# Optimization experiments

Hardware: AMD Instinct MI355X
Metric: run time of the kernel (lower is better)

The kernel has to match this reference:

```python
import jax, jax.numpy as jnp
import numpy as np

EPS = 1e-20  # MaskSoftmax epsilon
S, T, B, H, V = 64, 64, 128, 1024, 32000


def _attn(s, h, u, mask, sa_w, sa_b, a1_w, a1_b):
    # Bahdanau attention with mask-softmax over the source (dim 0)
    t = jnp.tanh(s @ sa_w + sa_b + u)               # [S,B,H]
    e = jnp.einsum('sbh,h->sb', t, a1_w) + a1_b     # [S,B]
    x = jnp.exp(e - jnp.max(e, axis=0, keepdims=True)) * mask
    alpha = x / (jnp.sum(x, axis=0, keepdims=True) + EPS)
    return jnp.einsum('sb,sbh->bh', alpha, h)       # [B,H]


def _gru(x, h, ym, W, U, b, C=None, c=None):
    xg = x @ W + b
    if C is not None:
        xg = xg + c @ C
    hg = h @ U
    xz, xr, xh = jnp.split(xg, 3, axis=-1)
    hz, hr, hh = jnp.split(hg, 3, axis=-1)
    z = jax.nn.sigmoid(xz + hz)
    r = jax.nn.sigmoid(xr + hr)
    hn = (1.0 - z) * h + z * jnp.tanh(xh + r * hh)
    m = ym[:, None]
    return m * hn + (1.0 - m) * h


def _forward(ys, xs_h, uh, xs_mask, ys_mask, s_tm1, emb, sa_w, sa_b, a1_w, a1_b,
             ha_w, ha_b, W1, U1, b1, W2, U2, C2, b2,
             ua1_w, ua1_b, ua2_w, ua2_b, ls_w, ls_b, ly_w, ly_b, lc_w, lc_b):
    ys_e = emb[ys]                                              # [T,B,H]
    btg_uh = jnp.einsum('sbh,hk->sbk', xs_h, ha_w) + ha_b        # [S,B,H]

    def step(s, inp):
        y_e, ym = inp
        s_above = _gru(y_e, s, ym, W1, U1, b1)                   # gru1
        a1 = _attn(s_above, xs_h, uh, xs_mask, sa_w, sa_b, a1_w, a1_b)
        a2 = _attn(s_above, xs_h, btg_uh, xs_mask, sa_w, sa_b, a1_w, a1_b)
        s_t = _gru(a1, s_above, ym, W2, U2, b2, C2, a2)          # gru2 with extra ctx
        g = jax.nn.sigmoid(a1 @ ua1_w + ua1_b + a2 @ ua2_w + ua2_b)
        att = g * a1 + (1.0 - g) * a2                            # gated fusion
        logit = s_t @ ls_w + ls_b + y_e @ ly_w + ly_b + att @ lc_w + lc_b  # [B,2H]
        logit = jnp.max(logit.reshape(logit.shape[0], -1, 2), axis=-1)     # maxout
        return s_t, logit

    _, logits = jax.lax.scan(step, s_tm1, (ys_e, ys_mask))       # [T,B,H]
    return logits * ys_mask[:, :, None]


def setup_inputs():
    key = jax.random.key(0)
    ks = jax.random.split(key, 20)
    rn = lambda k, sh, s=0.02: jax.random.normal(k, sh, jnp.float32) * s
    inp = {}
    inp['ys'] = jax.random.randint(ks[0], (T, B), 0, V)
    inp['xs_h'] = jax.random.normal(ks[1], (S, B, H), jnp.float32)
    inp['uh'] = jax.random.normal(ks[2], (S, B, H), jnp.float32)
    inp['xs_mask'] = jnp.ones((S, B), jnp.float32)
    inp['ys_mask'] = jnp.ones((T, B), jnp.float32)
    inp['s_tm1'] = rn(ks[3], (B, H), 1.0)
    emb = rn(ks[4], (V, H), 1.0)
    inp['emb'] = emb.at[0].set(0.0)  # padding_idx = 0
    inp['sa_w'] = rn(ks[5], (H, H)); inp['sa_b'] = jnp.zeros((H,), jnp.float32)
    inp['a1_w'] = rn(ks[6], (H,));   inp['a1_b'] = jnp.zeros((), jnp.float32)
    inp['ha_w'] = rn(ks[7], (H, H)); inp['ha_b'] = jnp.zeros((H,), jnp.float32)
    inp['W1'] = rn(ks[8], (H, 3 * H)); inp['U1'] = rn(ks[9], (H, 3 * H)); inp['b1'] = jnp.zeros((3 * H,), jnp.float32)
    inp['W2'] = rn(ks[10], (H, 3 * H)); inp['U2'] = rn(ks[11], (H, 3 * H)); inp['C2'] = rn(ks[12], (H, 3 * H)); inp['b2'] = jnp.zeros((3 * H,), jnp.float32)
    inp['ua1_w'] = rn(ks[13], (H, H)); inp['ua1_b'] = jnp.zeros((H,), jnp.float32)
    inp['ua2_w'] = rn(ks[14], (H, H)); inp['ua2_b'] = jnp.zeros((H,), jnp.float32)
    inp['ls_w'] = rn(ks[15], (H, 2 * H)); inp['ls_b'] = jnp.zeros((2 * H,), jnp.float32)
    inp['ly_w'] = rn(ks[16], (H, 2 * H)); inp['ly_b'] = jnp.zeros((2 * H,), jnp.float32)
    inp['lc_w'] = rn(ks[17], (H, 2 * H)); inp['lc_b'] = jnp.zeros((2 * H,), jnp.float32)
    return inp


def reference(ys, xs_h, uh, xs_mask, ys_mask, s_tm1, emb, sa_w, sa_b, a1_w, a1_b,
              ha_w, ha_b, W1, U1, b1, W2, U2, C2, b2,
              ua1_w, ua1_b, ua2_w, ua2_b, ls_w, ls_b, ly_w, ly_b, lc_w, lc_b):
    return _forward(ys, xs_h, uh, xs_mask, ys_mask, s_tm1, emb, sa_w, sa_b, a1_w, a1_b,
                    ha_w, ha_b, W1, U1, b1, W2, U2, C2, b2,
                    ua1_w, ua1_b, ua2_w, ua2_b, ls_w, ls_b, ly_w, ly_b, lc_w, lc_b)
```

## Files before the change

### kernel.cpp

```cpp
#include <hip/hip_runtime.h>
#include <hip/hip_bf16.h>
#include <cstddef>
#include <cstdint>

#define Sdim 64
#define Tdim 64
#define Bdim 128
#define Hdim 1024
#define H3 3072
#define TB (Tdim * Bdim)
#define SB (Sdim * Bdim)
#define NWG 256

typedef __attribute__((ext_vector_type(4))) float f32x4;
typedef __attribute__((ext_vector_type(8))) short bf16x8;

__device__ __forceinline__ float rcpf(float x) { return __builtin_amdgcn_rcpf(x); }
__device__ __forceinline__ float sigf(float x) { return rcpf(1.0f + __expf(-x)); }
__device__ __forceinline__ float tanh_fast(float x) {
  x = fminf(fmaxf(x, -15.0f), 15.0f);
  float t = __expf(2.0f * x);
  return (t - 1.0f) * rcpf(t + 1.0f);
}
__device__ __forceinline__ float bl(uint32_t u) { return __uint_as_float(u << 16); }
__device__ __forceinline__ float bh(uint32_t u) { return __uint_as_float(u & 0xffff0000u); }
__device__ __forceinline__ float b2f(uint16_t v) { return __uint_as_float((uint32_t)v << 16); }
__device__ __forceinline__ uint16_t f2b(float f) {
  __hip_bfloat16 h = __float2bfloat16(f);
  return *reinterpret_cast<uint16_t*>(&h);
}

__device__ __forceinline__ uint32_t ald32(const void* p) {
  return __hip_atomic_load((const uint32_t*)p, __ATOMIC_RELAXED, __HIP_MEMORY_SCOPE_AGENT);
}
__device__ __forceinline__ unsigned long long ald64(const void* p) {
  return __hip_atomic_load((const unsigned long long*)p, __ATOMIC_RELAXED, __HIP_MEMORY_SCOPE_AGENT);
}
__device__ __forceinline__ void ast32(void* p, uint32_t v) {
  __hip_atomic_store((uint32_t*)p, v, __ATOMIC_RELAXED, __HIP_MEMORY_SCOPE_AGENT);
}
__device__ __forceinline__ void ast64(void* p, unsigned long long v) {
  __hip_atomic_store((unsigned long long*)p, v, __ATOMIC_RELAXED, __HIP_MEMORY_SCOPE_AGENT);
}
__device__ __forceinline__ float aldf(const void* p) { return __uint_as_float(ald32(p)); }
__device__ __forceinline__ void astf(void* p, float v) { ast32(p, __float_as_uint(v)); }
__device__ __forceinline__ uint4 ald128(const void* p) {
  unsigned long long a = ald64(p);
  unsigned long long b = ald64((const char*)p + 8);
  uint4 r;
  r.x = (uint32_t)a; r.y = (uint32_t)(a >> 32);
  r.z = (uint32_t)b; r.w = (uint32_t)(b >> 32);
  return r;
}
#define PK2(x, y) ((unsigned long long)__float_as_uint(x) | ((unsigned long long)__float_as_uint(y) << 32))
__device__ __forceinline__ float ulo(unsigned long long u) { return __uint_as_float((uint32_t)u); }
__device__ __forceinline__ float uhi(unsigned long long u) { return __uint_as_float((uint32_t)(u >> 32)); }

struct MDesc {
  const uint16_t* A0; const uint16_t* B0;
  const uint16_t* A1; const uint16_t* B1;
  const uint16_t* A2; const uint16_t* B2;
  const float* bias0; const float* bias1; const float* bias2;
  float* C;
  int M, N, K;
};

template<int BM, int BN, int MODE>
__global__ __launch_bounds__(256) void mgemm(MDesc d, const float* __restrict__ ymask,
                                             float* __restrict__ outp)
{
  const int nb = blockIdx.x * BN;
  const int mb = blockIdx.y * BM;
  if (nb >= d.N || mb >= d.M) return;

  __shared__ char lds[(BM + BN) * 128];
  char* As = lds;
  char* Bs = lds + BM * 128;

  const int t = threadIdx.x;
  const int lane = t & 63;
  const int wid = t >> 6;
  const int wm = wid >> 1, wn = wid & 1;
  constexpr int WM = BM / 2, WN = BN / 2;
  constexpr int MR = WM / 16, NR = WN / 16;
  constexpr int CA = BM / 32;
  constexpr int CB = BN / 32;

  const int arow_base = wm * WM + (lane & 15);
  const int brow_base = wn * WN + (lane & 15);
  const int akb = (lane >> 4) * 16;
  const int axA = (arow_base & 7) << 4;
  const int axB = (brow_base & 7) << 4;

  f32x4 acc[MR][NR];
  #pragma unroll
  for (int m = 0; m < MR; ++m)
    #pragma unroll
    for (int n = 0; n < NR; ++n)
      acc[m][n] = (f32x4){0.f, 0.f, 0.f, 0.f};

  const int K = d.K;
  const int nkt = K / 64;

  #pragma unroll 1
  for (int p = 0; p < 3; ++p) {
    const uint16_t* A = (p == 0) ? d.A0 : (p == 1 ? d.A1 : d.A2);
    const uint16_t* B = (p == 0) ? d.B0 : (p == 1 ? d.B1 : d.B2);
    if (A == nullptr) break;

    const char* gA[CA]; int lA[CA];
    const char* gB[CB]; int lB[CB];
    #pragma unroll
    for (int c = 0; c < CA; ++c) {
      int i = c * 256 + t, row = i >> 3, kb = (i & 7) * 16;
      gA[c] = (const char*)A + (size_t)(mb + row) * K * 2 + kb;
      lA[c] = row * 128 + (kb ^ ((row & 7) << 4));
    }
    #pragma unroll
    for (int c = 0; c < CB; ++c) {
      int i = c * 256 + t, row = i >> 3, kb = (i & 7) * 16;
      gB[c] = (const char*)B + (size_t)(nb + row) * K * 2 + kb;
      lB[c] = row * 128 + (kb ^ ((row & 7) << 4));
    }

    uint4 ra[CA], rb[CB];
    #pragma unroll
    for (int c = 0; c < CA; ++c) ra[c] = *(const uint4*)gA[c];
    #pragma unroll
    for (int c = 0; c < CB; ++c) rb[c] = *(const uint4*)gB[c];

    for (int kk = 0; kk < nkt; ++kk) {
      __syncthreads();
      #pragma unroll
      for (int c = 0; c < CA; ++c) *(uint4*)(As + lA[c]) = ra[c];
      #pragma unroll
      for (int c = 0; c < CB; ++c) *(uint4*)(Bs + lB[c]) = rb[c];
      __syncthreads();
      if (kk + 1 < nkt) {
        #pragma unroll
        for (int c = 0; c < CA; ++c) ra[c] = *(const uint4*)(gA[c] + (size_t)(kk + 1) * 128);
        #pragma unroll
        for (int c = 0; c < CB; ++c) rb[c] = *(const uint4*)(gB[c] + (size_t)(kk + 1) * 128);
      }
      #pragma unroll
      for (int ks = 0; ks < 2; ++ks) {
        bf16x8 av[MR], bv[NR];
        #pragma unroll
        for (int m = 0; m < MR; ++m) {
          int row = arow_base + m * 16;
          av[m] = *(const bf16x8*)(As + row * 128 + ((ks * 64 + akb) ^ axA));
        }
        #pragma unroll
        for (int n = 0; n < NR; ++n) {
          int row = brow_base + n * 16;
          bv[n] = *(const bf16x8*)(Bs + row * 128 + ((ks * 64 + akb) ^ axB));
        }
        #pragma unroll
        for (int m = 0; m < MR; ++m)
          #pragma unroll
          for (int n = 0; n < NR; ++n)
            acc[m][n] = __builtin_amdgcn_mfma_f32_16x16x32_bf16(av[m], bv[n], acc[m][n], 0, 0, 0);
      }
    }
  }

  const int cm = (lane >> 4) * 4;
  const int cn = lane & 15;
  #pragma unroll
  for (int n = 0; n < NR; ++n) {
    int col = nb + wn * WN + n * 16 + cn;
    float bias = 0.f;
    if (d.bias0) bias += d.bias0[col];
    if (d.bias1) bias += d.bias1[col];
    if (d.bias2) bias += d.bias2[col];
    #pragma unroll
    for (int m = 0; m < MR; ++m) {
      #pragma unroll
      for (int j = 0; j < 4; ++j) {
        int row = mb + wm * WM + m * 16 + cm + j;
        float v = acc[m][n][j] + bias;
        if (MODE == 1) {
          ((uint16_t*)d.C)[(size_t)row * d.N + col] = f2b(v);
        } else {
          float o = __shfl_xor(v, 1);
          if (!(lane & 1))
            outp[(size_t)row * (d.N / 2) + (col >> 1)] = fmaxf(v, o) * ymask[row];
        }
      }
    }
  }
}

static inline MDesc mk(const uint16_t* A0, const uint16_t* B0,
                       const uint16_t* A1, const uint16_t* B1,
                       const uint16_t* A2, const uint16_t* B2,
                       const float* b0, const float* b1, const float* b2,
                       float* C, int M, int N, int K)
{
  MDesc d;
  d.A0 = A0; d.B0 = B0; d.A1 = A1; d.B1 = B1; d.A2 = A2; d.B2 = B2;
  d.bias0 = b0; d.bias1 = b1; d.bias2 = b2;
  d.C = C; d.M = M; d.N = N; d.K = K;
  return d;
}

__global__ __launch_bounds__(256) void transpose_bf16_k(const float* __restrict__ in,
                                                        uint16_t* __restrict__ out,
                                                        int K, int N)
{
  __shared__ float tile[32][33];
  int nx = blockIdx.x * 32, ky = blockIdx.y * 32;
  int tx = threadIdx.x & 31, ty = threadIdx.x >> 5;
  #pragma unroll
  for (int i = 0; i < 4; ++i)
    tile[ty + i * 8][tx] = in[(size_t)(ky + ty + i * 8) * N + nx + tx];
  __syncthreads();
  #pragma unroll
  for (int i = 0; i < 4; ++i)
    out[(size_t)(nx + ty + i * 8) * K + ky + tx] = f2b(tile[tx][ty + i * 8]);
}

__global__ __launch_bounds__(256) void ptranspose_k(const float* __restrict__ in,
                                                    uint16_t* __restrict__ out,
                                                    int K, int N)
{
  __shared__ float tile[32][33];
  int nx = blockIdx.x * 32, ky = blockIdx.y * 32;
  int tx = threadIdx.x & 31, ty = threadIdx.x >> 5;
  #pragma unroll
  for (int i = 0; i < 4; ++i)
    tile[ty + i * 8][tx] = in[(size_t)(ky + ty + i * 8) * N + nx + tx];
  __syncthreads();
  #pragma unroll
  for (int i = 0; i < 4; ++i) {
    int n = nx + ty + i * 8;
    int h = n & 1023, g = n >> 10;
    int np = (h >> 4) * 48 + g * 16 + (h & 15);
    out[(size_t)np * K + ky + tx] = f2b(tile[tx][ty + i * 8]);
  }
}

__global__ __launch_bounds__(256) void pack_k(const float* __restrict__ b1,
                                              const float* __restrict__ b2,
                                              float* __restrict__ b1p,
                                              float* __restrict__ b2p,
                                              int* __restrict__ bar)
{
  int i = blockIdx.x * 256 + threadIdx.x;
  if (i < 1024) bar[i] = 0;
  if (i < H3) {
    int g = (i >> 4) % 3, hblk = i / 48, hi = i & 15;
    int n = g * 1024 + hblk * 16 + hi;
    b1p[i] = b1[n];
    b2p[i] = b2[n];
  }
}

__global__ __launch_bounds__(256) void cvt_bf16_k(const float* __restrict__ in,
                                                  uint16_t* __restrict__ out)
{
  int gid = blockIdx.x * 256 + threadIdx.x;
  float4 v = ((const float4*)in)[gid];
  uint2 o;
  o.x = (uint32_t)f2b(v.x) | ((uint32_t)f2b(v.y) << 16);
  o.y = (uint32_t)f2b(v.z) | ((uint32_t)f2b(v.w) << 16);
  ((uint2*)out)[gid] = o;
}

__global__ __launch_bounds__(256) void embed_k(const int* __restrict__ ys,
                                               const float* __restrict__ emb,
                                               uint16_t* __restrict__ ys_e)
{
  int gid = blockIdx.x * 256 + threadIdx.x;
  int h4 = gid & 255;
  int tb = gid >> 8;
  int tok = ys[tb];
  float4 v = ((const float4*)emb)[(size_t)tok * 256 + h4];
  uint2 o;
  o.x = (uint32_t)f2b(v.x) | ((uint32_t)f2b(v.y) << 16);
  o.y = (uint32_t)f2b(v.z) | ((uint32_t)f2b(v.w) << 16);
  ((uint2*)ys_e)[gid] = o;
}

struct ScanArgs {
  const uint16_t *U1p, *W2p, *C2p, *U2p;
  const uint16_t *sawt, *ua1t, *ua2t;
  const uint16_t *xw1p;
  const uint16_t *uh_bf, *btg_bf, *xs_bf;
  const uint16_t *stm1_bf;
  const float *s_tm1, *ys_mask, *xs_mask, *a1w, *a1b, *sa_b;
  const float *b2p, *ua1_b, *ua2_b;
  float *sf0, *sf1, *sab_f, *qbuf, *e1, *e2, *c1f, *c2f, *ahg;
  float *p1part, *p5part;
  uint16_t *sab_bf, *c1b, *c2b, *shist_bf, *att_bf;
  int *bar;
};

__device__ __forceinline__ void gsync(int* bar, int gen, int wg) {
  __syncthreads();
  if (threadIdx.x == 0) {
    asm volatile("s_waitcnt vmcnt(0)" ::: "memory");
    int old = __hip_atomic_fetch_add(bar + (wg & 15) * 32, 1,
                                     __ATOMIC_RELAXED, __HIP_MEMORY_SCOPE_AGENT);
    if (old == gen * 16 - 1) {
      int ro = __hip_atomic_fetch_add(bar + 512, 1,
                                      __ATOMIC_RELAXED, __HIP_MEMORY_SCOPE_AGENT);
      if (ro == gen * 16 - 1)
        __hip_atomic_store(bar + 544, gen, __ATOMIC_RELAXED, __HIP_MEMORY_SCOPE_AGENT);
    }
    while (__hip_atomic_load(bar + 544, __ATOMIC_RELAXED, __HIP_MEMORY_SCOPE_AGENT) < gen)
      __builtin_amdgcn_s_sleep(2);
    asm volatile("s_waitcnt vmcnt(0)" ::: "memory");
  }
  __syncthreads();
}

#define HS1 16384
#define HS2 12288
#define HS6 16384
#define HS5 32768


__global__ __launch_bounds__(256, 1) void scan2_k(ScanArgs a) {
  const int wg = blockIdx.x;
  const int t = threadIdx.x;
  const int lane = t & 63, w = t >> 6;
  const int r15 = lane & 15;
  const int akb = (lane >> 4) * 16;
  __shared__ char lds[64 * 1024];
  int gen = 0;

  float wv[16];
  {
    const float* wp = a.a1w + lane * 16;
    #pragma unroll
    for (int j = 0; j < 16; ++j) wv[j] = wp[j];
  }
  const float abv = a.a1b[0];

  const int b34 = wg & 127;
  const uint16_t* src34 = (wg < 128) ? a.uh_bf : a.btg_bf;
  const size_t s34_base = ((size_t)(w * 16) * Bdim + b34) * 1024 + lane * 16;
  float* cf34 = (wg < 128) ? a.c1f : a.c2f;
  uint16_t* cb34 = (wg < 128) ? a.c1b : a.c2b;
  const uint16_t* xp34 = a.xs_bf + (size_t)b34 * 1024 + t * 4;

  const int bh6 = (wg & 127) >> 6, hb6 = wg & 63;
  const char* ga6[4]; int la6[4];
  {
    #pragma unroll
    for (int c = 0; c < 4; ++c) {
      int i = c * 256 + t;
      int row = i >> 3, kb = (i & 7) * 16;
      if (i < 512) {
        ga6[c] = (const char*)a.sab_bf + ((size_t)(bh6 * 64 + row) * 1024) * 2 + kb;
      } else if (i < 896) {
        int j2 = i - 512; int row2 = j2 >> 3;
        ga6[c] = (const char*)a.U2p + ((size_t)(hb6 * 48 + row2) * 1024) * 2 + kb;
        row = 64 + row2;
      } else {
        ga6[c] = (const char*)a.U2p + kb;
      }
      la6[c] = row * 128 + (kb ^ ((row & 7) << 4));
    }
  }

  const int bh5 = (wg & 127) >> 6, hblk = wg & 63;
  const int pairid = wg & 127;
  const int koff = (wg < 128) ? 0 : 8;

  const char* ga5[8]; int la5[8];
  {
    #pragma unroll
    for (int c = 0; c < 8; ++c) {
      int i = c * 256 + t;
      int kb = (i & 7) * 16, grow = i >> 3;
      const char* gp;
      if (grow < 64)       gp = (const char*)a.c1b  + ((size_t)(bh5 * 64 + grow)        * 1024) * 2;
      else if (grow < 128) gp = (const char*)a.c2b  + ((size_t)(bh5 * 64 + grow - 64)   * 1024) * 2;
      else if (grow < 176) gp = (const char*)a.W2p  + ((size_t)(hblk * 48 + grow - 128) * 1024) * 2;
      else if (grow < 224) gp = (const char*)a.C2p  + ((size_t)(hblk * 48 + grow - 176) * 1024) * 2;
      else if (grow < 240) gp = (const char*)a.ua1t + ((size_t)(hblk * 16 + grow - 224) * 1024) * 2;
      else                 gp = (const char*)a.ua2t + ((size_t)(hblk * 16 + grow - 240) * 1024) * 2;
      ga5[c] = gp + kb + (size_t)koff * 128;
      la5[c] = grow * 128 + (kb ^ ((grow & 7) << 4));
    }
  }

  unsigned long long* p1p = (unsigned long long*)a.p1part + (size_t)pairid * 1536 + t;
  unsigned long long* p5p = (unsigned long long*)a.p5part + (size_t)pairid * 2048 + t;

  for (int step = 0; step < Tdim; ++step) {
    const uint16_t* sprev_bf = step ? (a.shist_bf + (size_t)(step - 1) * Bdim * Hdim) : a.stm1_bf;
    const float* sprev_f = (step == 0) ? a.s_tm1 : ((step & 1) ? a.sf0 : a.sf1);
    float* snext_f = (step & 1) ? a.sf1 : a.sf0;
    const float* ymt = a.ys_mask + (size_t)step * Bdim;
    uint16_t* shist_t = a.shist_bf + (size_t)step * Bdim * Hdim;
    uint16_t* att_t = a.att_bf + (size_t)step * Bdim * Hdim;
    const uint16_t* xw1t = a.xw1p + (size_t)step * Bdim * H3;

    {
      const char* ga1[4]; int la1[4];
      #pragma unroll
      for (int c = 0; c < 4; ++c) {
        int i = c * 256 + t;
        int row = i >> 3, kb = (i & 7) * 16;
        if (i < 512) {
          ga1[c] = (const char*)sprev_bf + ((size_t)(bh5 * 64 + row) * 1024) * 2 + kb;
        } else if (i < 896) {
          int j2 = i - 512; int row2 = j2 >> 3;
          ga1[c] = (const char*)a.U1p + ((size_t)(hblk * 48 + row2) * 1024) * 2 + kb;
          row = 64 + row2;
        } else {
          ga1[c] = (const char*)a.U1p + kb;
        }
        ga1[c] += (size_t)koff * 128;
        la1[c] = row * 128 + (kb ^ ((row & 7) << 4));
      }
      f32x4 ac0 = {0.f,0.f,0.f,0.f}, ac1 = ac0, ac2 = ac0;
      const int arow = w * 16 + r15;
      const int axA = (arow & 7) << 4;
      const int axB = (r15 & 7) << 4;
      uint4 rA[4], rB[4];
      auto ld1 = [&](uint4* r, int tile) {
        #pragma unroll
        for (int c = 0; c < 4; ++c)
          r[c] = (c < 2) ? ald128(ga1[c] + (size_t)tile * 128)
                         : *(const uint4*)(ga1[c] + (size_t)tile * 128);
      };
      auto st1 = [&](const uint4* r, int half) {
        char* base = lds + half * HS1;
        #pragma unroll
        for (int c = 0; c < 4; ++c) *(uint4*)(base + la1[c]) = r[c];
      };
      auto cp1 = [&](int half) {
        const char* base = lds + half * HS1;
        #pragma unroll
        for (int ks = 0; ks < 2; ++ks) {
          int ko = ks * 64 + akb;
          bf16x8 av = *(const bf16x8*)(base + arow * 128 + (ko ^ axA));
          bf16x8 b0 = *(const bf16x8*)(base + (64 + r15) * 128 + (ko ^ axB));
          bf16x8 b1 = *(const bf16x8*)(base + (80 + r15) * 128 + (ko ^ axB));
          bf16x8 b2 = *(const bf16x8*)(base + (96 + r15) * 128 + (ko ^ axB));
          ac0 = __builtin_amdgcn_mfma_f32_16x16x32_bf16(av, b0, ac0, 0, 0, 0);
          ac1 = __builtin_amdgcn_mfma_f32_16x16x32_bf16(av, b1, ac1, 0, 0, 0);
          ac2 = __builtin_amdgcn_mfma_f32_16x16x32_bf16(av, b2, ac2, 0, 0, 0);
        }
      };
      ld1(rA, 0); ld1(rB, 1);
      st1(rA, 0);
      #pragma unroll 1
      for (int kk2 = 0; kk2 < 4; ++kk2) {
        __syncthreads();
        st1(rB, 1);
        if (kk2 < 3) ld1(rA, 2 * kk2 + 2);
        cp1(0);
        __syncthreads();
        if (kk2 < 3) { st1(rA, 0); ld1(rB, 2 * kk2 + 3); }
        cp1(1);
      }
      if (wg >= 128) {
        ast64(p1p +    0, PK2(ac0[0], ac0[1]));
        ast64(p1p +  256, PK2(ac0[2], ac0[3]));
        ast64(p1p +  512, PK2(ac1[0], ac1[1]));
        ast64(p1p +  768, PK2(ac1[2], ac1[3]));
        ast64(p1p + 1024, PK2(ac2[0], ac2[1]));
        ast64(p1p + 1280, PK2(ac2[2], ac2[3]));
        __syncthreads();
        if (t == 0)
          __hip_atomic_store(a.bar + 600 + pairid, step + 1,
                             __ATOMIC_RELAXED, __HIP_MEMORY_SCOPE_AGENT);
      } else {
        if (t == 0) {
          while (__hip_atomic_load(a.bar + 600 + pairid,
                                   __ATOMIC_RELAXED, __HIP_MEMORY_SCOPE_AGENT) < step + 1)
            __builtin_amdgcn_s_sleep(1);
        }
        __syncthreads();
        unsigned long long u0 = ald64(p1p), u1 = ald64(p1p + 256),
                           u2 = ald64(p1p + 512), u3 = ald64(p1p + 768),
                           u4 = ald64(p1p + 1024), u5 = ald64(p1p + 1280);
        ac0[0] += ulo(u0); ac0[1] += uhi(u0); ac0[2] += ulo(u1); ac0[3] += uhi(u1);
        ac1[0] += ulo(u2); ac1[1] += uhi(u2); ac1[2] += ulo(u3); ac1[3] += uhi(u3);
        ac2[0] += ulo(u4); ac2[1] += uhi(u4); ac2[2] += ulo(u5); ac2[3] += uhi(u5);
        const int hgl = hblk * 16 + r15;
        const int bbase = bh5 * 64 + w * 16 + ((lane >> 4) << 2);
        #pragma unroll
        for (int j = 0; j < 4; ++j) {
          int b = bbase + j;
          size_t xr_ = (size_t)b * H3 + hblk * 48 + r15;
          float xz = b2f(xw1t[xr_]);
          float xr = b2f(xw1t[xr_ + 16]);
          float xh = b2f(xw1t[xr_ + 32]);
          float hp = aldf(sprev_f + b * 1024 + hgl);
          float z = sigf(xz + ac0[j]);
          float r = sigf(xr + ac1[j]);
          float hn = (1.f - z) * hp + z * tanh_fast(xh + r * ac2[j]);
          float m = ymt[b];
          float o = m * hn + (1.f - m) * hp;
          astf(a.sab_f + b * 1024 + hgl, o);
          uint32_t me = f2b(o);
          uint32_t other = (uint32_t)__shfl_xor((int)me, 1);
          if (!(lane & 1))
            ast32((char*)a.sab_bf + ((size_t)b * 1024 + hgl) * 2, me | (other << 16));
        }
      }
    }
    gsync(a.bar, ++gen, wg);

    if (wg < 64) {
      const int bh2 = wg >> 5, nblk = wg & 31;
      const char* ga2[3]; int la2[3];
      #pragma unroll
      for (int c = 0; c < 3; ++c) {
        int i = c * 256 + t;
        int row, kb = (i & 7) * 16;
        if (i < 512) {
          row = i >> 3;
          ga2[c] = (const char*)a.sab_bf + ((size_t)(bh2 * 64 + row) * 1024) * 2 + kb;
        } else {
          int j2 = i - 512; int row2 = j2 >> 3;
          ga2[c] = (const char*)a.sawt + ((size_t)(nblk * 32 + row2) * 1024) * 2 + kb;
          row = 64 + row2;
        }
        la2[c] = row * 128 + (kb ^ ((row & 7) << 4));
      }
      f32x4 q0 = {0.f,0.f,0.f,0.f}, q1 = q0;
      const int arow = w * 16 + r15;
      const int axA = (arow & 7) << 4;
      const int axB = (r15 & 7) << 4;
      uint4 rA[3], rB[3];
      auto ld2 = [&](uint4* r, int tile) {
        #pragma unroll
        for (int c = 0; c < 3; ++c)
          r[c] = (c < 2) ? ald128(ga2[c] + (size_t)tile * 128)
                         : *(const uint4*)(ga2[c] + (size_t)tile * 128);
      };
      auto st2 = [&](const uint4* r, int half) {
        char* base = lds + half * HS2;
        #pragma unroll
        for (int c = 0; c < 3; ++c) *(uint4*)(base + la2[c]) = r[c];
      };
      auto cp2 = [&](int half) {
        const char* base = lds + half * HS2;
        #pragma unroll
        for (int ks = 0; ks < 2; ++ks) {
          int ko = ks * 64 + akb;
          bf16x8 av = *(const bf16x8*)(base + arow * 128 + (ko ^ axA));
          bf16x8 b0 = *(const bf16x8*)(base + (64 + r15) * 128 + (ko ^ axB));
          bf16x8 b1 = *(const bf16x8*)(base + (80 + r15) * 128 + (ko ^ axB));
          q0 = __builtin_amdgcn_mfma_f32_16x16x32_bf16(av, b0, q0, 0, 0, 0);
          q1 = __builtin_amdgcn_mfma_f32_16x16x32_bf16(av, b1, q1, 0, 0, 0);
        }
      };
      ld2(rA, 0); ld2(rB, 1);
      st2(rA, 0);
      #pragma unroll 1
      for (int kk2 = 0; kk2 < 8; ++kk2) {
        __syncthreads();
        st2(rB, 1);
        if (kk2 < 7) ld2(rA, 2 * kk2 + 2);
        cp2(0);
        __syncthreads();
        if (kk2 < 7) { st2(rA, 0); ld2(rB, 2 * kk2 + 3); }
        cp2(1);
      }
      #pragma unroll
      for (int n = 0; n < 2; ++n) {
        int col = nblk * 32 + n * 16 + r15;
        float sb = a.sa_b[col];
        #pragma unroll
        for (int j = 0; j < 4; ++j) {
          int b = bh2 * 64 + w * 16 + ((lane >> 4) << 2) + j;
          astf(a.qbuf + b * 1024 + col, (n ? q1[j] : q0[j]) + sb);
        }
      }
    } else if (wg >= 128) {
      f32x4 ac0 = {0.f,0.f,0.f,0.f}, ac1 = ac0, ac2 = ac0;
      const int arow = w * 16 + r15;
      const int axA = (arow & 7) << 4;
      const int axB = (r15 & 7) << 4;
      uint4 rA[4], rB[4];
      auto ld6 = [&](uint4* r, int tile) {
        #pragma unroll
        for (int c = 0; c < 4; ++c)
          r[c] = (c < 2) ? ald128(ga6[c] + (size_t)tile * 128)
                         : *(const uint4*)(ga6[c] + (size_t)tile * 128);
      };
      auto st6 = [&](const uint4* r, int half) {
        char* base = lds + half * HS6;
        #pragma unroll
        for (int c = 0; c < 4; ++c) *(uint4*)(base + la6[c]) = r[c];
      };
      auto cp6 = [&](int half) {
        const char* base = lds + half * HS6;
        #pragma unroll
        for (int ks = 0; ks < 2; ++ks) {
          int ko = ks * 64 + akb;
          bf16x8 av = *(const bf16x8*)(base + arow * 128 + (ko ^ axA));
          bf16x8 b0 = *(const bf16x8*)(base + (64 + r15) * 128 + (ko ^ axB));
          bf16x8 b1 = *(const bf16x8*)(base + (80 + r15) * 128 + (ko ^ axB));
          bf16x8 b2 = *(const bf16x8*)(base + (96 + r15) * 128 + (ko ^ axB));
          ac0 = __builtin_amdgcn_mfma_f32_16x16x32_bf16(av, b0, ac0, 0, 0, 0);
          ac1 = __builtin_amdgcn_mfma_f32_16x16x32_bf16(av, b1, ac1, 0, 0, 0);
          ac2 = __builtin_amdgcn_mfma_f32_16x16x32_bf16(av, b2, ac2, 0, 0, 0);
        }
      };
      ld6(rA, 0); ld6(rB, 1);
      st6(rA, 0);
      #pragma unroll 1
      for (int kk2 = 0; kk2 < 8; ++kk2) {
        __syncthreads();
        st6(rB, 1);
        if (kk2 < 7) ld6(rA, 2 * kk2 + 2);
        cp6(0);
        __syncthreads();
        if (kk2 < 7) { st6(rA, 0); ld6(rB, 2 * kk2 + 3); }
        cp6(1);
      }
      const int bbase6 = bh6 * 64 + w * 16 + ((lane >> 4) << 2);
      #pragma unroll
      for (int j = 0; j < 4; ++j) {
        int b = bbase6 + j;
        float* ap = a.ahg + (size_t)b * H3 + hb6 * 48 + r15;
        astf(ap, ac0[j]);
        astf(ap + 16, ac1[j]);
        astf(ap + 32, ac2[j]);
      }
    }
    uint4 pa0 = *(const uint4*)(src34 + s34_base);
    uint4 pa1 = *(const uint4*)(src34 + s34_base + 8);
    gsync(a.bar, ++gen, wg);

    {
      float* e_lds = (float*)lds;
      float qv[16];
      const float* qp = a.qbuf + (size_t)b34 * 1024 + lane * 16;
      #pragma unroll
      for (int k2 = 0; k2 < 8; ++k2) {
        unsigned long long q2 = ald64(qp + k2 * 2);
        qv[2 * k2]     = __uint_as_float((uint32_t)q2);
        qv[2 * k2 + 1] = __uint_as_float((uint32_t)(q2 >> 32));
      }
      auto score = [&](uint4 u0, uint4 u1, int si) {
        float pv = 0.f;
        uint32_t uu[8] = {u0.x,u0.y,u0.z,u0.w,u1.x,u1.y,u1.z,u1.w};
        #pragma unroll
        for (int k = 0; k < 8; ++k) {
          pv += wv[2*k]   * tanh_fast(qv[2*k]   + bl(uu[k]));
          pv += wv[2*k+1] * tanh_fast(qv[2*k+1] + bh(uu[k]));
        }
        #pragma unroll
        for (int off = 32; off > 0; off >>= 1) pv += __shfl_xor(pv, off);
        if (lane == 0) e_lds[w * 16 + si] = pv + abv;
      };
      uint4 pb0, pb1;
      {
        const uint16_t* np = src34 + s34_base + (size_t)Bdim * 1024;
        pb0 = *(const uint4*)np; pb1 = *(const uint4*)(np + 8);
      }
      #pragma unroll 1
      for (int s2 = 0; s2 < 8; ++s2) {
        {
          int si = 2 * s2;
          uint4 u0 = pa0, u1 = pa1;
          if (s2 < 7) {
            const uint16_t* np = src34 + s34_base + (size_t)(si + 2) * Bdim * 1024;
            pa0 = *(const uint4*)np; pa1 = *(const uint4*)(np + 8);
          }
          score(u0, u1, si);
        }
        {
          int si = 2 * s2 + 1;
          uint4 u0 = pb0, u1 = pb1;
          if (s2 < 7) {
            const uint16_t* np = src34 + s34_base + (size_t)(si + 2) * Bdim * 1024;
            pb0 = *(const uint4*)np; pb1 = *(const uint4*)(np + 8);
          }
          score(u0, u1, si);
        }
      }
      __syncthreads();
      if (w == 0) {
        float vv = e_lds[lane];
        float mx = vv;
        #pragma unroll
        for (int off = 32; off > 0; off >>= 1) mx = fmaxf(mx, __shfl_xor(mx, off));
        float x = __expf(vv - mx) * a.xs_mask[lane * Bdim + b34];
        float sm = x;
        #pragma unroll
        for (int off = 32; off > 0; off >>= 1) sm += __shfl_xor(sm, off);
        e_lds[lane] = x * rcpf(sm + 1e-20f);
      }
      __syncthreads();
      float s0 = 0.f, s1 = 0.f, s2 = 0.f, s3 = 0.f;
      #pragma unroll 8
      for (int s = 0; s < Sdim; ++s) {
        unsigned long long u = *(const unsigned long long*)(xp34 + (size_t)s * Bdim * 1024);
        float aa = e_lds[s];
        s0 += aa * bl((uint32_t)u);
        s1 += aa * bh((uint32_t)u);
        s2 += aa * bl((uint32_t)(u >> 32));
        s3 += aa * bh((uint32_t)(u >> 32));
      }
      size_t o = (size_t)b34 * 1024 + t * 4;
      ast64(cf34 + o,     (unsigned long long)__float_as_uint(s0)
                        | ((unsigned long long)__float_as_uint(s1) << 32));
      ast64(cf34 + o + 2, (unsigned long long)__float_as_uint(s2)
                        | ((unsigned long long)__float_as_uint(s3) << 32));
      unsigned long long pb = (unsigned long long)f2b(s0)
                            | ((unsigned long long)f2b(s1) << 16)
                            | ((unsigned long long)f2b(s2) << 32)
                            | ((unsigned long long)f2b(s3) << 48);
      ast64((char*)cb34 + o * 2, pb);
    }
    uint4 v5w[8];
    {
      #pragma unroll
      for (int c = 4; c < 8; ++c) {
        v5w[c - 4] = *(const uint4*)ga5[c];
        v5w[c]     = *(const uint4*)(ga5[c] + 128);
      }
    }
    gsync(a.bar, ++gen, wg);

    {
      f32x4 ax0 = {0.f,0.f,0.f,0.f}, ax1 = ax0, ax2 = ax0, ag = ax0;
      uint4 rA[8], rB[8];
      auto ld5 = [&](uint4* r, int tile) {
        #pragma unroll
        for (int c = 0; c < 8; ++c)
          r[c] = (c < 4) ? ald128(ga5[c] + (size_t)tile * 128)
                         : *(const uint4*)(ga5[c] + (size_t)tile * 128);
      };
      auto st5 = [&](const uint4* r, int half) {
        char* base = lds + half * HS5;
        #pragma unroll
        for (int c = 0; c < 8; ++c) *(uint4*)(base + la5[c]) = r[c];
      };
      auto cp5 = [&](int half) {
        const char* base = lds + half * HS5;
        #pragma unroll
        for (int ks = 0; ks < 2; ++ks) {
          const int ko = ks * 64 + akb;
          #define LD(row_) (*(const bf16x8*)(base + (row_) * 128 + (ko ^ (((row_) & 7) << 4))))
          bf16x8 a1v = LD(w * 16 + r15);
          bf16x8 a2v = LD(64 + w * 16 + r15);
          bf16x8 bw0 = LD(128 + r15), bw1 = LD(144 + r15), bw2 = LD(160 + r15);
          bf16x8 bc0 = LD(176 + r15), bc1 = LD(192 + r15), bc2 = LD(208 + r15);
          bf16x8 g1v = LD(224 + r15), g2v = LD(240 + r15);
          #undef LD
          ax0 = __builtin_amdgcn_mfma_f32_16x16x32_bf16(a1v, bw0, ax0, 0, 0, 0);
          ax0 = __builtin_amdgcn_mfma_f32_16x16x32_bf16(a2v, bc0, ax0, 0, 0, 0);
          ax1 = __builtin_amdgcn_mfma_f32_16x16x32_bf16(a1v, bw1, ax1, 0, 0, 0);
          ax1 = __builtin_amdgcn_mfma_f32_16x16x32_bf16(a2v, bc1, ax1, 0, 0, 0);
          ax2 = __builtin_amdgcn_mfma_f32_16x16x32_bf16(a1v, bw2, ax2, 0, 0, 0);
          ax2 = __builtin_amdgcn_mfma_f32_16x16x32_bf16(a2v, bc2, ax2, 0, 0, 0);
          ag  = __builtin_amdgcn_mfma_f32_16x16x32_bf16(a1v, g1v, ag, 0, 0, 0);
          ag  = __builtin_amdgcn_mfma_f32_16x16x32_bf16(a2v, g2v, ag, 0, 0, 0);
        }
      };
      #pragma unroll
      for (int c = 0; c < 4; ++c) {
        rA[c] = ald128(ga5[c]);
        rB[c] = ald128(ga5[c] + 128);
      }
      #pragma unroll
      for (int c = 4; c < 8; ++c) { rA[c] = v5w[c - 4]; rB[c] = v5w[c]; }
      st5(rA, 0);
      #pragma unroll 1
      for (int kk2 = 0; kk2 < 4; ++kk2) {
        __syncthreads();
        st5(rB, 1);
        if (kk2 < 3) ld5(rA, 2 * kk2 + 2);
        cp5(0);
        __syncthreads();
        if (kk2 < 3) { st5(rA, 0); ld5(rB, 2 * kk2 + 3); }
        cp5(1);
      }
      if (wg >= 128) {
        ast64(p5p +    0, PK2(ax0[0], ax0[1]));
        ast64(p5p +  256, PK2(ax0[2], ax0[3]));
        ast64(p5p +  512, PK2(ax1[0], ax1[1]));
        ast64(p5p +  768, PK2(ax1[2], ax1[3]));
        ast64(p5p + 1024, PK2(ax2[0], ax2[1]));
        ast64(p5p + 1280, PK2(ax2[2], ax2[3]));
        ast64(p5p + 1536, PK2(ag[0], ag[1]));
        ast64(p5p + 1792, PK2(ag[2], ag[3]));
        __syncthreads();
        if (t == 0)
          __hip_atomic_store(a.bar + 728 + pairid, step + 1,
                             __ATOMIC_RELAXED, __HIP_MEMORY_SCOPE_AGENT);
      } else {
        if (t == 0) {
          while (__hip_atomic_load(a.bar + 728 + pairid,
                                   __ATOMIC_RELAXED, __HIP_MEMORY_SCOPE_AGENT) < step + 1)
            __builtin_amdgcn_s_sleep(1);
        }
        __syncthreads();
        unsigned long long u0 = ald64(p5p), u1 = ald64(p5p + 256),
                           u2 = ald64(p5p + 512), u3 = ald64(p5p + 768),
                           u4 = ald64(p5p + 1024), u5 = ald64(p5p + 1280),
                           u6 = ald64(p5p + 1536), u7 = ald64(p5p + 1792);
        ax0[0] += ulo(u0); ax0[1] += uhi(u0); ax0[2] += ulo(u1); ax0[3] += uhi(u1);
        ax1[0] += ulo(u2); ax1[1] += uhi(u2); ax1[2] += ulo(u3); ax1[3] += uhi(u3);
        ax2[0] += ulo(u4); ax2[1] += uhi(u4); ax2[2] += ulo(u5); ax2[3] += uhi(u5);
        ag[0]  += ulo(u6); ag[1]  += uhi(u6); ag[2]  += ulo(u7); ag[3]  += uhi(u7);
        const int hgl = hblk * 16 + r15;
        float bz  = a.b2p[hblk * 48 + r15];
        float brr = a.b2p[hblk * 48 + 16 + r15];
        float bhh = a.b2p[hblk * 48 + 32 + r15];
        float gb  = a.ua1_b[hgl] + a.ua2_b[hgl];
        const int bbase = bh5 * 64 + w * 16 + ((lane >> 4) << 2);
        float ahz[4], ahr[4], ahh[4], hpv[4], c1v[4], c2v[4];
        #pragma unroll
        for (int j = 0; j < 4; ++j) {
          int b = bbase + j;
          const float* ap = a.ahg + (size_t)b * H3 + hblk * 48 + r15;
          ahz[j] = aldf(ap);
          ahr[j] = aldf(ap + 16);
          ahh[j] = aldf(ap + 32);
          hpv[j] = aldf(a.sab_f + (size_t)b * 1024 + hgl);
          c1v[j] = aldf(a.c1f + (size_t)b * 1024 + hgl);
          c2v[j] = aldf(a.c2f + (size_t)b * 1024 + hgl);
        }
        #pragma unroll
        for (int j = 0; j < 4; ++j) {
          int b = bbase + j;
          float hp = hpv[j];
          float z = sigf(ax0[j] + bz + ahz[j]);
          float r = sigf(ax1[j] + brr + ahr[j]);
          float hn = (1.f - z) * hp + z * tanh_fast(ax2[j] + bhh + r * ahh[j]);
          float m = ymt[b];
          float st = m * hn + (1.f - m) * hp;
          astf(snext_f + b * 1024 + hgl, st);
          uint32_t me = f2b(st);
          uint32_t other = (uint32_t)__shfl_xor((int)me, 1);
          if (!(lane & 1))
            ast32((char*)shist_t + ((size_t)b * 1024 + hgl) * 2, me | (other << 16));
          float g = sigf(ag[j] + gb);
          float att = g * c1v[j] + (1.f - g) * c2v[j];
          att_t[(size_t)b * 1024 + hgl] = f2b(att);
        }
      }
    }
    gsync(a.bar, ++gen, wg);
  }
}

extern "C" void kernel_launch(void* const* d_in, const int* in_sizes, int n_in,
                              void* d_out, int out_size, void* d_ws, size_t ws_size,
                              hipStream_t stream)
{
  const int*   ys      = (const int*)  d_in[0];
  const float* xs_h    = (const float*)d_in[1];
  const float* uh      = (const float*)d_in[2];
  const float* xs_mask = (const float*)d_in[3];
  const float* ys_mask = (const float*)d_in[4];
  const float* s_tm1   = (const float*)d_in[5];
  const float* emb     = (const float*)d_in[6];
  const float* sa_w    = (const float*)d_in[7];
  const float* sa_b    = (const float*)d_in[8];
  const float* a1_w    = (const float*)d_in[9];
  const float* a1_b    = (const float*)d_in[10];
  const float* ha_w    = (const float*)d_in[11];
  const float* ha_b    = (const float*)d_in[12];
  const float* W1      = (const float*)d_in[13];
  const float* U1      = (const float*)d_in[14];
  const float* b1      = (const float*)d_in[15];
  const float* W2      = (const float*)d_in[16];
  const float* U2      = (const float*)d_in[17];
  const float* C2      = (const float*)d_in[18];
  const float* b2      = (const float*)d_in[19];
  const float* ua1_w   = (const float*)d_in[20];
  const float* ua1_b   = (const float*)d_in[21];
  const float* ua2_w   = (const float*)d_in[22];
  const float* ua2_b   = (const float*)d_in[23];
  const float* ls_w    = (const float*)d_in[24];
  const float* ls_b    = (const float*)d_in[25];
  const float* ly_w    = (const float*)d_in[26];
  const float* ly_b    = (const float*)d_in[27];
  const float* lc_w    = (const float*)d_in[28];
  const float* lc_b    = (const float*)d_in[29];
  (void)in_sizes; (void)n_in; (void)out_size; (void)ws_size;

  float* out = (float*)d_out;

  char* wp = (char*)d_ws;
  auto alloc = [&](size_t bytes) { char* r = wp; wp += (bytes + 255) & ~(size_t)255; return r; };

  uint16_t* W1p  = (uint16_t*)alloc((size_t)H3 * Hdim * 2);
  uint16_t* U1p  = (uint16_t*)alloc((size_t)H3 * Hdim * 2);
  uint16_t* W2p  = (uint16_t*)alloc((size_t)H3 * Hdim * 2);
  uint16_t* U2p  = (uint16_t*)alloc((size_t)H3 * Hdim * 2);
  uint16_t* C2p  = (uint16_t*)alloc((size_t)H3 * Hdim * 2);
  uint16_t* sawt = (uint16_t*)alloc((size_t)Hdim * Hdim * 2);
  uint16_t* hawt = (uint16_t*)alloc((size_t)Hdim * Hdim * 2);
  uint16_t* ua1t = (uint16_t*)alloc((size_t)Hdim * Hdim * 2);
  uint16_t* ua2t = (uint16_t*)alloc((size_t)Hdim * Hdim * 2);
  uint16_t* lst  = (uint16_t*)alloc((size_t)2048 * Hdim * 2);
  uint16_t* lyt  = (uint16_t*)alloc((size_t)2048 * Hdim * 2);
  uint16_t* lct  = (uint16_t*)alloc((size_t)2048 * Hdim * 2);
  float* b1p = (float*)alloc((size_t)H3 * 4);
  float* b2p = (float*)alloc((size_t)H3 * 4);
  int* bar   = (int*)alloc(4096);
  uint16_t* uh_bf   = (uint16_t*)alloc((size_t)SB * Hdim * 2);
  uint16_t* xs_bf   = (uint16_t*)alloc((size_t)SB * Hdim * 2);
  uint16_t* btg_bf  = (uint16_t*)alloc((size_t)SB * Hdim * 2);
  uint16_t* ys_e_bf = (uint16_t*)alloc((size_t)TB * Hdim * 2);
  uint16_t* xw1p    = (uint16_t*)alloc((size_t)TB * H3 * 2);
  uint16_t* shist_bf= (uint16_t*)alloc((size_t)TB * Hdim * 2);
  uint16_t* att_bf  = (uint16_t*)alloc((size_t)TB * Hdim * 2);
  uint16_t* stm1_bf = (uint16_t*)alloc((size_t)Bdim * Hdim * 2);
  float* sab_f = (float*)alloc((size_t)Bdim * Hdim * 4);
  uint16_t* sab_bf = (uint16_t*)alloc((size_t)Bdim * Hdim * 2);
  float* qbuf = (float*)alloc((size_t)Bdim * Hdim * 4);
  float* c1f  = (float*)alloc((size_t)Bdim * Hdim * 4);
  float* c2f  = (float*)alloc((size_t)Bdim * Hdim * 4);
  uint16_t* c1b = (uint16_t*)alloc((size_t)Bdim * Hdim * 2);
  uint16_t* c2b = (uint16_t*)alloc((size_t)Bdim * Hdim * 2);
  float* e1 = (float*)alloc((size_t)SB * 4);
  float* e2 = (float*)alloc((size_t)SB * 4);
  float* sf0 = (float*)alloc((size_t)Bdim * Hdim * 4);
  float* sf1 = (float*)alloc((size_t)Bdim * Hdim * 4);
  float* ahg = (float*)alloc((size_t)Bdim * H3 * 4);
  float* p1part = (float*)alloc((size_t)128 * 1536 * 8);
  float* p5part = (float*)alloc((size_t)128 * 2048 * 8);

  pack_k<<<12, 256, 0, stream>>>(b1, b2, b1p, b2p, bar);

  auto ptr3 = [&](const float* in, uint16_t* o) {
    ptranspose_k<<<dim3(H3 / 32, Hdim / 32), 256, 0, stream>>>(in, o, Hdim, H3);
  };
  ptr3(W1, W1p); ptr3(U1, U1p); ptr3(W2, W2p); ptr3(U2, U2p); ptr3(C2, C2p);

  auto tr = [&](const float* in, uint16_t* o, int K, int N) {
    transpose_bf16_k<<<dim3(N / 32, K / 32), 256, 0, stream>>>(in, o, K, N);
  };
  tr(sa_w, sawt, Hdim, Hdim); tr(ha_w, hawt, Hdim, Hdim);
  tr(ua1_w, ua1t, Hdim, Hdim); tr(ua2_w, ua2t, Hdim, Hdim);
  tr(ls_w, lst, Hdim, 2048); tr(ly_w, lyt, Hdim, 2048); tr(lc_w, lct, Hdim, 2048);

  cvt_bf16_k<<<(SB * Hdim / 4) / 256, 256, 0, stream>>>(uh, uh_bf);
  cvt_bf16_k<<<(SB * Hdim / 4) / 256, 256, 0, stream>>>(xs_h, xs_bf);
  cvt_bf16_k<<<(Bdim * Hdim / 4) / 256, 256, 0, stream>>>(s_tm1, stm1_bf);
  embed_k<<<(TB * Hdim / 4) / 256, 256, 0, stream>>>(ys, emb, ys_e_bf);

  {
    MDesc d = mk(ys_e_bf, W1p, 0, 0, 0, 0, b1p, 0, 0, (float*)xw1p, TB, H3, Hdim);
    mgemm<128, 128, 1><<<dim3(H3 / 128, TB / 128), 256, 0, stream>>>(d, nullptr, nullptr);
  }
  {
    MDesc d = mk(xs_bf, hawt, 0, 0, 0, 0, ha_b, 0, 0, (float*)btg_bf, SB, Hdim, Hdim);
    mgemm<128, 128, 1><<<dim3(Hdim / 128, SB / 128), 256, 0, stream>>>(d, nullptr, nullptr);
  }

  ScanArgs sa;
  sa.U1p = U1p; sa.W2p = W2p; sa.C2p = C2p; sa.U2p = U2p;
  sa.sawt = sawt; sa.ua1t = ua1t; sa.ua2t = ua2t;
  sa.xw1p = xw1p;
  sa.uh_bf = uh_bf; sa.btg_bf = btg_bf; sa.xs_bf = xs_bf;
  sa.stm1_bf = stm1_bf;
  sa.s_tm1 = s_tm1; sa.ys_mask = ys_mask; sa.xs_mask = xs_mask;
  sa.a1w = a1_w; sa.a1b = a1_b; sa.sa_b = sa_b;
  sa.b2p = b2p; sa.ua1_b = ua1_b; sa.ua2_b = ua2_b;
  sa.sf0 = sf0; sa.sf1 = sf1; sa.sab_f = sab_f; sa.qbuf = qbuf;
  sa.e1 = e1; sa.e2 = e2; sa.c1f = c1f; sa.c2f = c2f; sa.ahg = ahg;
  sa.p1part = p1part; sa.p5part = p5part;
  sa.sab_bf = sab_bf; sa.c1b = c1b; sa.c2b = c2b;
  sa.shist_bf = shist_bf; sa.att_bf = att_bf;
  sa.bar = bar;
  scan2_k<<<NWG, 256, 0, stream>>>(sa);

  {
    MDesc d = mk(shist_bf, lst, ys_e_bf, lyt, att_bf, lct, ls_b, ly_b, lc_b,
                 nullptr, TB, 2048, Hdim);
    mgemm<128, 128, 2><<<dim3(2048 / 128, TB / 128), 256, 0, stream>>>(d, ys_mask, out);
  }
}
```

Before: 4.966 ms.

## Cache per-batch attention keys in LDS across scan steps via dynamic shared memory

Each persistent workgroup now loads its batch column of uh/btg (64 source rows of 1024 bf16, 128KB) into dynamic LDS once before the time loop. The attention score loop then reads keys from LDS instead of re-fetching them from global memory every step. GEMM staging moves to a 32KB region after the cache, and the stage-5 pipeline drops from double buffering to single buffering with extra barriers. The risk is that 160KB of LDS and the lost overlap in stage 5 slow the other phases.

```diff
diff --git a/kernel.cpp b/kernel.cpp
--- a/kernel.cpp
+++ b/kernel.cpp
@@ -315,19 +315,20 @@
   __syncthreads();
 }
 
+#define STRCACHE 131072
 #define HS1 16384
 #define HS2 12288
 #define HS6 16384
-#define HS5 32768
 
 
 __global__ __launch_bounds__(256, 1) void scan2_k(ScanArgs a) {
+  extern __shared__ char lds[];
+  char* stg = lds + STRCACHE;
   const int wg = blockIdx.x;
   const int t = threadIdx.x;
   const int lane = t & 63, w = t >> 6;
   const int r15 = lane & 15;
   const int akb = (lane >> 4) * 16;
-  __shared__ char lds[64 * 1024];
   int gen = 0;
 
   float wv[16];
@@ -340,10 +341,20 @@
 
   const int b34 = wg & 127;
   const uint16_t* src34 = (wg < 128) ? a.uh_bf : a.btg_bf;
-  const size_t s34_base = ((size_t)(w * 16) * Bdim + b34) * 1024 + lane * 16;
   float* cf34 = (wg < 128) ? a.c1f : a.c2f;
   uint16_t* cb34 = (wg < 128) ? a.c1b : a.c2b;
   const uint16_t* xp34 = a.xs_bf + (size_t)b34 * 1024 + t * 4;
+
+  {
+    #pragma unroll
+    for (int c = 0; c < 32; ++c) {
+      int idx = c * 256 + t;
+      int s = idx >> 7, hc = idx & 127;
+      const uint16_t* gp = src34 + ((size_t)(s * Bdim + b34)) * 1024 + hc * 8;
+      *(uint4*)(lds + s * 2048 + hc * 16) = *(const uint4*)gp;
+    }
+    __syncthreads();
+  }
 
   const int bh6 = (wg & 127) >> 6, hb6 = wg & 63;
   const char* ga6[4]; int la6[4];
@@ -429,12 +440,12 @@
                          : *(const uint4*)(ga1[c] + (size_t)tile * 128);
       };
       auto st1 = [&](const uint4* r, int half) {
-        char* base = lds + half * HS1;
+        char* base = stg + half * HS1;
         #pragma unroll
         for (int c = 0; c < 4; ++c) *(uint4*)(base + la1[c]) = r[c];
       };
       auto cp1 = [&](int half) {
-        const char* base = lds + half * HS1;
+        const char* base = stg + half * HS1;
         #pragma unroll
         for (int ks = 0; ks < 2; ++ks) {
           int ko = ks * 64 + akb;
@@ -537,12 +548,12 @@
                          : *(const uint4*)(ga2[c] + (size_t)tile * 128);
       };
       auto st2 = [&](const uint4* r, int half) {
-        char* base = lds + half * HS2;
+        char* base = stg + half * HS2;
         #pragma unroll
         for (int c = 0; c < 3; ++c) *(uint4*)(base + la2[c]) = r[c];
       };
       auto cp2 = [&](int half) {
-        const char* base = lds + half * HS2;
+        const char* base = stg + half * HS2;
         #pragma unroll
         for (int ks = 0; ks < 2; ++ks) {
           int ko = ks * 64 + akb;
@@ -588,12 +599,12 @@
                          : *(const uint4*)(ga6[c] + (size_t)tile * 128);
       };
       auto st6 = [&](const uint4* r, int half) {
-        char* base = lds + half * HS6;
+        char* base = stg + half * HS6;
         #pragma unroll
         for (int c = 0; c < 4; ++c) *(uint4*)(base + la6[c]) = r[c];
       };
       auto cp6 = [&](int half) {
-        const char* base = lds + half * HS6;
+        const char* base = stg + half * HS6;
         #pragma unroll
         for (int ks = 0; ks < 2; ++ks) {
           int ko = ks * 64 + akb;
@@ -628,12 +639,10 @@
         astf(ap + 32, ac2[j]);
       }
     }
-    uint4 pa0 = *(const uint4*)(src34 + s34_base);
-    uint4 pa1 = *(const uint4*)(src34 + s34_base + 8);
     gsync(a.bar, ++gen, wg);
 
     {
-      float* e_lds = (float*)lds;
+      float* e_lds = (float*)stg;
       float qv[16];
       const float* qp = a.qbuf + (size_t)b34 * 1024 + lane * 16;
       #pragma unroll
@@ -642,7 +651,12 @@
         qv[2 * k2]     = __uint_as_float((uint32_t)q2);
         qv[2 * k2 + 1] = __uint_as_float((uint32_t)(q2 >> 32));
       }
-      auto score = [&](uint4 u0, uint4 u1, int si) {
+      #pragma unroll 1
+      for (int si = 0; si < 16; ++si) {
+        int srow = w * 16 + si;
+        const char* cpp = lds + srow * 2048 + lane * 32;
+        uint4 u0 = *(const uint4*)cpp;
+        uint4 u1 = *(const uint4*)(cpp + 16);
         float pv = 0.f;
         uint32_t uu[8] = {u0.x,u0.y,u0.z,u0.w,u1.x,u1.y,u1.z,u1.w};
         #pragma unroll
@@ -652,33 +666,7 @@
         }
         #pragma unroll
         for (int off = 32; off > 0; off >>= 1) pv += __shfl_xor(pv, off);
-        if (lane == 0) e_lds[w * 16 + si] = pv + abv;
-      };
-      uint4 pb0, pb1;
-      {
-        const uint16_t* np = src34 + s34_base + (size_t)Bdim * 1024;
-        pb0 = *(const uint4*)np; pb1 = *(const uint4*)(np + 8);
-      }
-      #pragma unroll 1
-      for (int s2 = 0; s2 < 8; ++s2) {
-        {
-          int si = 2 * s2;
-          uint4 u0 = pa0, u1 = pa1;
-          if (s2 < 7) {
-            const uint16_t* np = src34 + s34_base + (size_t)(si + 2) * Bdim * 1024;
-            pa0 = *(const uint4*)np; pa1 = *(const uint4*)(np + 8);
-          }
-          score(u0, u1, si);
-        }
-        {
-          int si = 2 * s2 + 1;
-          uint4 u0 = pb0, u1 = pb1;
-          if (s2 < 7) {
-            const uint16_t* np = src34 + s34_base + (size_t)(si + 2) * Bdim * 1024;
-            pb0 = *(const uint4*)np; pb1 = *(const uint4*)(np + 8);
-          }
-          score(u0, u1, si);
-        }
+        if (lane == 0) e_lds[srow] = pv + abv;
       }
       __syncthreads();
       if (w == 0) {
@@ -733,13 +721,12 @@
           r[c] = (c < 4) ? ald128(ga5[c] + (size_t)tile * 128)
                          : *(const uint4*)(ga5[c] + (size_t)tile * 128);
       };
-      auto st5 = [&](const uint4* r, int half) {
-        char* base = lds + half * HS5;
-        #pragma unroll
-        for (int c = 0; c < 8; ++c) *(uint4*)(base + la5[c]) = r[c];
-      };
-      auto cp5 = [&](int half) {
-        const char* base = lds + half * HS5;
+      auto st5 = [&](const uint4* r) {
+        #pragma unroll
+        for (int c = 0; c < 8; ++c) *(uint4*)(stg + la5[c]) = r[c];
+      };
+      auto cp5 = [&]() {
+        const char* base = stg;
         #pragma unroll
         for (int ks = 0; ks < 2; ++ks) {
           const int ko = ks * 64 + akb;
@@ -767,16 +754,18 @@
       }
       #pragma unroll
       for (int c = 4; c < 8; ++c) { rA[c] = v5w[c - 4]; rB[c] = v5w[c]; }
-      st5(rA, 0);
       #pragma unroll 1
-      for (int kk2 = 0; kk2 < 4; ++kk2) {
-        __syncthreads();
-        st5(rB, 1);
-        if (kk2 < 3) ld5(rA, 2 * kk2 + 2);
-        cp5(0);
-        __syncthreads();
-        if (kk2 < 3) { st5(rA, 0); ld5(rB, 2 * kk2 + 3); }
-        cp5(1);
+      for (int k2 = 0; k2 < 4; ++k2) {
+        __syncthreads();
+        st5(rA);
+        __syncthreads();
+        if (k2 < 3) ld5(rA, 2 * k2 + 2);
+        cp5();
+        __syncthreads();
+        st5(rB);
+        __syncthreads();
+        if (k2 < 3) ld5(rB, 2 * k2 + 3);
+        cp5();
       }
       if (wg >= 128) {
         ast64(p5p +    0, PK2(ax0[0], ax0[1]));
@@ -955,6 +944,12 @@
     mgemm<128, 128, 1><<<dim3(Hdim / 128, SB / 128), 256, 0, stream>>>(d, nullptr, nullptr);
   }
 
+  static bool attr_set = false;
+  if (!attr_set) {
+    hipFuncSetAttribute((const void*)scan2_k,
+                        hipFuncAttributeMaxDynamicSharedMemorySize, 163840);
+    attr_set = true;
+  }
   ScanArgs sa;
   sa.U1p = U1p; sa.W2p = W2p; sa.C2p = C2p; sa.U2p = U2p;
   sa.sawt = sawt; sa.ua1t = ua1t; sa.ua2t = ua2t;
@@ -970,7 +965,7 @@
   sa.sab_bf = sab_bf; sa.c1b = c1b; sa.c2b = c2b;
   sa.shist_bf = shist_bf; sa.att_bf = att_bf;
   sa.bar = bar;
-  scan2_k<<<NWG, 256, 0, stream>>>(sa);
+  scan2_k<<<NWG, 256, 163840, stream>>>(sa);
 
   {
     MDesc d = mk(shist_bf, lst, ys_e_bf, lyt, att_bf, lct, ls_b, ly_b, lc_b,
```

After: 4.893 ms. About the same (-1.5%).
